# Kernel tuning notes

Measured on AMD Instinct MI355X. Metric: run time of the kernel, lower is better.

## Reference

```python
import jax, jax.numpy as jnp
import numpy as np

B, S, H = 1, 2048, 2048
NH = 16
HS = H // NH  # 128
NEG = -65504.0  # fp16 min used as additive mask value


def setup_inputs() -> dict:
    key = jax.random.key(0)
    k1, k2, k3, k4, k5 = jax.random.split(key, 5)
    hidden_states = jax.random.normal(k1, (B, S, H), dtype=jnp.float32)
    # causal left-to-right mask: 1 where attention allowed
    ltor_mask = jnp.tril(jnp.ones((S, S), dtype=jnp.float32))[None, None, :, :]
    W_qkv = jax.random.normal(k2, (H, 3 * H), dtype=jnp.float32) * (1.0 / np.sqrt(H))
    b_qkv = jax.random.normal(k3, (3 * H,), dtype=jnp.float32) * 0.01
    W_dense = jax.random.normal(k4, (H, H), dtype=jnp.float32) * (1.0 / np.sqrt(H))
    b_dense = jax.random.normal(k5, (H,), dtype=jnp.float32) * 0.01
    return {"hidden_states": hidden_states, "ltor_mask": ltor_mask,
            "W_qkv": W_qkv, "b_qkv": b_qkv, "W_dense": W_dense, "b_dense": b_dense}


def reference(hidden_states, ltor_mask, W_qkv, b_qkv, W_dense, b_dense):
    b, s, h = hidden_states.shape
    # fused QKV projection, then split along last dim (matches split_tensor_along_last_dim)
    qkv = hidden_states @ W_qkv + b_qkv  # [b, s, 3h]
    q, k, v = jnp.split(qkv, 3, axis=-1)
    q = q.reshape(b, s, NH, HS)
    k = k.reshape(b, s, NH, HS)
    v = v.reshape(b, s, NH, HS)
    scale = 1.0 / np.sqrt(HS)  # softmax_scale=None -> 1/sqrt(headdim)
    scores = jnp.einsum('bqhd,bkhd->bhqk', q, k) * scale
    scores = scores + NEG * (1.0 - ltor_mask)  # additive mask, [b,1,s,s] broadcast over heads
    probs = jax.nn.softmax(scores, axis=-1)
    ctx = jnp.einsum('bhqk,bkhd->bqhd', probs, v).reshape(b, s, h)
    out = ctx @ W_dense + b_dense  # output_dropout is identity in eval
    return out
```

## Files before the change

### kernel.cpp

```cpp
#include <hip/hip_runtime.h>
#include <math.h>

#define S_LEN 2048
#define HDIM  2048
#define NHEAD 16
#define HSZ   128
#define H3    6144

typedef __attribute__((ext_vector_type(8))) short bf16x8;
typedef __attribute__((ext_vector_type(4))) float f32x4;

__device__ inline ushort f2bf(float f) {
    union { float f; unsigned u; } c; c.f = f;
    unsigned u = c.u;
    return (ushort)((u + 0x7fffu + ((u >> 16) & 1u)) >> 16);
}
__device__ inline ushort f2bf_trunc(float f) {
    union { float f; unsigned u; } c; c.f = f;
    return (ushort)(c.u >> 16);
}

__global__ __launch_bounds__(256) void prep(
    const float* __restrict__ X,    ushort* __restrict__ Xb,
    const float* __restrict__ Wqkv, ushort* __restrict__ Wqt,
    const float* __restrict__ Wd,   ushort* __restrict__ Wdt)
{
    __shared__ ushort t[64][66];
    const int bid = blockIdx.x;
    const int tid = threadIdx.x;

    if (bid < 4096) {
        int i = bid * 1024 + tid * 4;
        float4 v = *(const float4*)(X + i);
        ushort4 o;
        o.x = f2bf(v.x); o.y = f2bf(v.y); o.z = f2bf(v.z); o.w = f2bf(v.w);
        *(ushort4*)(Xb + i) = o;
        return;
    }

    const float* W; ushort* Wt; int K, N, n0, k0;
    if (bid < 7168) {
        const int b = bid - 4096;
        W = Wqkv; Wt = Wqt; K = HDIM; N = H3;
        n0 = (b % 96) * 64; k0 = (b / 96) * 64;
    } else {
        const int b = bid - 7168;
        W = Wd; Wt = Wdt; K = HDIM; N = HDIM;
        n0 = (b % 32) * 64; k0 = (b / 32) * 64;
    }
    const int tx = tid & 15;
    const int ty = tid >> 4;
    #pragma unroll
    for (int p = 0; p < 4; p++) {
        const int k = p * 16 + ty;
        float4 v = *(const float4*)(&W[(size_t)(k0 + k) * N + n0 + tx * 4]);
        t[k][tx * 4 + 0] = f2bf(v.x);
        t[k][tx * 4 + 1] = f2bf(v.y);
        t[k][tx * 4 + 2] = f2bf(v.z);
        t[k][tx * 4 + 3] = f2bf(v.w);
    }
    __syncthreads();
    #pragma unroll
    for (int p = 0; p < 4; p++) {
        const int n = p * 16 + ty;
        ushort4 o;
        o.x = t[tx * 4 + 0][n];
        o.y = t[tx * 4 + 1][n];
        o.z = t[tx * 4 + 2][n];
        o.w = t[tx * 4 + 3][n];
        *(ushort4*)(&Wt[(size_t)(n0 + n) * K + k0 + tx * 4]) = o;
    }
}

__global__ __launch_bounds__(256) void transpose_v(const ushort* __restrict__ qkvb,
                                                   ushort* __restrict__ Vtb) {
    __shared__ ushort t[64][66];
    const int s0 = blockIdx.x * 64;
    const int d0 = blockIdx.y * 64;
    const int tx = threadIdx.x & 15;
    const int ty = threadIdx.x >> 4;
    #pragma unroll
    for (int p = 0; p < 4; p++) {
        const int s = p * 16 + ty;
        ushort4 v = *(const ushort4*)(&qkvb[(size_t)(s0 + s) * H3 + 2 * HDIM + d0 + tx * 4]);
        *(ushort4*)(&t[s][tx * 4]) = v;
    }
    __syncthreads();
    #pragma unroll
    for (int p = 0; p < 4; p++) {
        const int d = p * 16 + ty;
        ushort4 o;
        o.x = t[tx * 4 + 0][d];
        o.y = t[tx * 4 + 1][d];
        o.z = t[tx * 4 + 2][d];
        o.w = t[tx * 4 + 3][d];
        *(ushort4*)(&Vtb[(size_t)(d0 + d) * S_LEN + s0 + tx * 4]) = o;
    }
}

__global__ __launch_bounds__(256, 2) void gemm_qkv_v4(
    const ushort* __restrict__ A, const ushort* __restrict__ Bt,
    const float* __restrict__ bias, ushort* __restrict__ Cb,
    int M, int N, int K)
{
    __shared__ __align__(16) ushort lds[2][128 * 64 + 192 * 64];

    const int tid  = threadIdx.x;
    const int m0   = blockIdx.y * 128;
    const int n0   = blockIdx.x * 192;
    const int w    = tid >> 6;
    const int wm   = w >> 1;
    const int wn   = w & 1;
    const int lane = tid & 63;
    const int quad = lane >> 4;
    const int l16  = lane & 15;

    const int rdsw = l16 & 7;

    f32x4 acc[4][6] = {};

    const int T = K / 64;

    auto stage = [&](int kt) {
        const int b  = kt & 1;
        const int k0 = kt * 64;
        #pragma unroll
        for (int r = 0; r < 4; r++) {
            const int c   = r * 256 + tid;
            const int row = c >> 3;
            const int csw = ((c & 7) ^ (row & 7)) * 8;
            const ushort* ga = A + (size_t)(m0 + row) * K + k0 + csw;
            __builtin_amdgcn_global_load_lds(
                (const __attribute__((address_space(1))) void*)ga,
                (__attribute__((address_space(3))) void*)(&lds[b][0] + c * 8), 16, 0, 0);
        }
        #pragma unroll
        for (int r = 0; r < 6; r++) {
            const int c   = r * 256 + tid;
            const int row = c >> 3;
            const int csw = ((c & 7) ^ (row & 7)) * 8;
            const ushort* gb = Bt + (size_t)(n0 + row) * K + k0 + csw;
            __builtin_amdgcn_global_load_lds(
                (const __attribute__((address_space(1))) void*)gb,
                (__attribute__((address_space(3))) void*)(&lds[b][8192] + c * 8), 16, 0, 0);
        }
    };

    stage(0);

    for (int u = 0; u < T; u++) {
        const int b = u & 1;
        if (u + 1 < T) {
            stage(u + 1);
            asm volatile("s_waitcnt vmcnt(10)" ::: "memory");
        } else {
            asm volatile("s_waitcnt vmcnt(0)" ::: "memory");
        }
        asm volatile("s_barrier" ::: "memory");

        const ushort* bA = &lds[b][0];
        const ushort* bB = &lds[b][8192];

        bf16x8 af[4][2], bq[6][2];
        #pragma unroll
        for (int i = 0; i < 4; i++)
            #pragma unroll
            for (int kc = 0; kc < 2; kc++)
                af[i][kc] = *(const bf16x8*)(bA + (wm * 64 + i * 16 + l16) * 64
                                               + ((((kc << 2) | quad) ^ rdsw) * 8));
        #pragma unroll
        for (int j = 0; j < 6; j++)
            #pragma unroll
            for (int kc = 0; kc < 2; kc++)
                bq[j][kc] = *(const bf16x8*)(bB + (wn * 96 + j * 16 + l16) * 64
                                               + ((((kc << 2) | quad) ^ rdsw) * 8));

        __builtin_amdgcn_s_setprio(1);
        #pragma unroll
        for (int i = 0; i < 4; i++)
            #pragma unroll
            for (int j = 0; j < 6; j++)
                #pragma unroll
                for (int kc = 0; kc < 2; kc++)
                    acc[i][j] = __builtin_amdgcn_mfma_f32_16x16x32_bf16(
                        af[i][kc], bq[j][kc], acc[i][j], 0, 0, 0);
        __builtin_amdgcn_s_setprio(0);

        asm volatile("s_waitcnt lgkmcnt(0)" ::: "memory");
        asm volatile("s_barrier" ::: "memory");
    }

    #pragma unroll
    for (int i = 0; i < 4; i++) {
        #pragma unroll
        for (int r = 0; r < 4; r++) {
            const int m = m0 + wm * 64 + i * 16 + quad * 4 + r;
            #pragma unroll
            for (int j = 0; j < 6; j++) {
                const int n = n0 + wn * 96 + j * 16 + l16;
                float v  = acc[i][j][r] + bias[n];
                float vp = __shfl_xor(v, 1, 64);
                unsigned both = (unsigned)f2bf(v) | ((unsigned)f2bf(vp) << 16);
                if ((l16 & 1) == 0)
                    *(unsigned*)(Cb + (size_t)m * N + n) = both;
            }
        }
    }
}

__global__ __launch_bounds__(256) void gemm_dense(
    const ushort* __restrict__ A, const ushort* __restrict__ Bt,
    const float* __restrict__ bias, float* __restrict__ C)
{
    __shared__ ushort sA[2 * 64 * 32];
    __shared__ ushort sB[2 * 128 * 32];

    const int tid  = threadIdx.x;
    const int m0   = blockIdx.y * 64;
    const int n0   = blockIdx.x * 128;
    const int w    = tid >> 6;
    const int lane = tid & 63;
    const int quad = lane >> 4;
    const int l16  = lane & 15;
    const int wr   = (w >> 1) * 32;
    const int wc   = (w & 1) * 64;

    f32x4 acc[2][4] = {};

    for (int k0 = 0; k0 < HDIM; k0 += 64) {
        #pragma unroll
        for (int iss = 0; iss < 2; iss++) {
            const int li  = iss * 256 + tid;
            const int c   = li >> 8;
            const int row = (li >> 2) & 63;
            const int kc  = (li & 3) * 8;
            const ushort* ga = A + (size_t)(m0 + row) * HDIM + k0 + c * 32 + kc;
            __builtin_amdgcn_global_load_lds(
                (const __attribute__((address_space(1))) void*)ga,
                (__attribute__((address_space(3))) void*)(sA + li * 8), 16, 0, 0);
        }
        #pragma unroll
        for (int iss = 0; iss < 4; iss++) {
            const int li  = iss * 256 + tid;
            const int c   = li >> 9;
            const int row = (li >> 2) & 127;
            const int kc  = (li & 3) * 8;
            const ushort* gb = Bt + (size_t)(n0 + row) * HDIM + k0 + c * 32 + kc;
            __builtin_amdgcn_global_load_lds(
                (const __attribute__((address_space(1))) void*)gb,
                (__attribute__((address_space(3))) void*)(sB + li * 8), 16, 0, 0);
        }
        __syncthreads();

        #pragma unroll
        for (int c = 0; c < 2; c++) {
            bf16x8 af[2], bq[4];
            #pragma unroll
            for (int i = 0; i < 2; i++)
                af[i] = *(const bf16x8*)(sA + c * 2048 + (wr + i * 16 + l16) * 32 + quad * 8);
            #pragma unroll
            for (int j = 0; j < 4; j++)
                bq[j] = *(const bf16x8*)(sB + c * 4096 + (wc + j * 16 + l16) * 32 + quad * 8);

            #pragma unroll
            for (int i = 0; i < 2; i++)
                #pragma unroll
                for (int j = 0; j < 4; j++)
                    acc[i][j] = __builtin_amdgcn_mfma_f32_16x16x32_bf16(
                        af[i], bq[j], acc[i][j], 0, 0, 0);
        }
        __syncthreads();
    }

    #pragma unroll
    for (int i = 0; i < 2; i++)
        #pragma unroll
        for (int r = 0; r < 4; r++) {
            const int m = m0 + wr + i * 16 + quad * 4 + r;
            #pragma unroll
            for (int j = 0; j < 4; j++) {
                const int n = n0 + wc + j * 16 + l16;
                C[(size_t)m * HDIM + n] = acc[i][j][r] + bias[n];
            }
        }
}

__global__ __launch_bounds__(256) void attn_split(
    const ushort* __restrict__ qkvb, const ushort* __restrict__ Vtb,
    float* __restrict__ po, float* __restrict__ ctxf)
{
    __shared__ __align__(16) ushort sK [2][64 * 128];
    __shared__ __align__(16) ushort sVt[2][128 * 64];
    __shared__ __align__(16) ushort Ps [4 * 1024];

    const int tid = threadIdx.x;
    const int bid = blockIdx.x;
    const int qt  = 31 - (bid >> 5);
    const int rem = bid & 31;
    const int h   = rem >> 1;
    const int sh  = rem & 1;
    const int nt  = qt + 1;
    const int h0  = (nt + 1) >> 1;
    const int ks  = sh ? h0 : 0;
    const int ke  = sh ? nt : h0;

    const int q0   = qt * 64;
    const int w    = tid >> 6;
    const int lane = tid & 63;
    const int quad = lane >> 4;
    const int l16  = lane & 15;
    const int qr0  = q0 + w * 16;

    const float scale = 0.08838834764831845f;

    bf16x8 qf[4];
    #pragma unroll
    for (int c = 0; c < 4; c++)
        qf[c] = *(const bf16x8*)(qkvb + (size_t)(qr0 + l16) * H3 + h * HSZ + c * 32 + quad * 8);

    f32x4 o[8] = {};
    float lsum[4] = {0.f, 0.f, 0.f, 0.f};

    const int skey = tid >> 2;
    const int sq8  = tid & 3;

    auto stage = [&](int kt, int b) {
        const int k0 = kt * 64;
        #pragma unroll
        for (int iss = 0; iss < 4; iss++) {
            const int li = iss * 256 + tid;
            const ushort* g = qkvb + (size_t)(k0 + skey) * H3 + HDIM + h * HSZ + iss * 32 + sq8 * 8;
            __builtin_amdgcn_global_load_lds(
                (const __attribute__((address_space(1))) void*)g,
                (__attribute__((address_space(3))) void*)(&sK[b][0] + li * 8), 16, 0, 0);
        }
        #pragma unroll
        for (int iss = 0; iss < 4; iss++) {
            const int li = iss * 256 + tid;
            const int c  = li >> 9;
            const int d  = (li >> 2) & 127;
            const ushort* g = Vtb + (size_t)(h * HSZ + d) * S_LEN + k0 + c * 32 + (li & 3) * 8;
            __builtin_amdgcn_global_load_lds(
                (const __attribute__((address_space(1))) void*)g,
                (__attribute__((address_space(3))) void*)(&sVt[b][0] + li * 8), 16, 0, 0);
        }
    };

    if (ks < ke) stage(ks, 0);
    const int wofs = w * 1024;

    for (int kt = ks; kt < ke; kt++) {
        const int b  = (kt - ks) & 1;
        const int k0 = kt * 64;

        if (kt + 1 < ke) {
            stage(kt + 1, b ^ 1);
            asm volatile("s_waitcnt vmcnt(8)" ::: "memory");
        } else {
            asm volatile("s_waitcnt vmcnt(0)" ::: "memory");
        }
        asm volatile("s_barrier" ::: "memory");

        const ushort* bK = &sK[b][0];
        const ushort* bV = &sVt[b][0];

        f32x4 sacc[4] = {};
        #pragma unroll
        for (int jt = 0; jt < 4; jt++)
            #pragma unroll
            for (int c = 0; c < 4; c++) {
                bf16x8 kf = *(const bf16x8*)(bK + c * 2048 + (jt * 16 + l16) * 32 + quad * 8);
                sacc[jt] = __builtin_amdgcn_mfma_f32_16x16x32_bf16(qf[c], kf, sacc[jt], 0, 0, 0);
            }

        float p[4][4];
        if (kt == qt) {
            #pragma unroll
            for (int jt = 0; jt < 4; jt++) {
                const int key = k0 + jt * 16 + l16;
                #pragma unroll
                for (int r = 0; r < 4; r++) {
                    float e = __expf(sacc[jt][r] * scale);
                    if (key > qr0 + quad * 4 + r) e = 0.f;
                    p[jt][r] = e;
                    lsum[r] += e;
                }
            }
        } else {
            #pragma unroll
            for (int jt = 0; jt < 4; jt++)
                #pragma unroll
                for (int r = 0; r < 4; r++) {
                    float e = __expf(sacc[jt][r] * scale);
                    p[jt][r] = e;
                    lsum[r] += e;
                }
        }

        #pragma unroll
        for (int jt = 0; jt < 4; jt++) {
            const int cpan = jt >> 1;
            const int lch  = (jt & 1) * 2 + (l16 >> 3);
            const int phys = lch ^ quad;
            #pragma unroll
            for (int r = 0; r < 4; r++) {
                const int row = quad * 4 + r;
                Ps[wofs + cpan * 512 + row * 32 + phys * 8 + (l16 & 7)] = f2bf_trunc(p[jt][r]);
            }
        }

        #pragma unroll
        for (int c = 0; c < 2; c++) {
            const int pph = quad ^ (l16 >> 2);
            bf16x8 pf = *(const bf16x8*)(Ps + wofs + c * 512 + l16 * 32 + pph * 8);
            #pragma unroll
            for (int ht = 0; ht < 8; ht++) {
                bf16x8 vf = *(const bf16x8*)(bV + c * 4096 + (ht * 16 + l16) * 32 + quad * 8);
                o[ht] = __builtin_amdgcn_mfma_f32_16x16x32_bf16(pf, vf, o[ht], 0, 0, 0);
            }
        }

        asm volatile("s_waitcnt lgkmcnt(0)" ::: "memory");
        asm volatile("s_barrier" ::: "memory");
    }

    float* poS = po + (size_t)sh * S_LEN * HDIM;

    #pragma unroll
    for (int r = 0; r < 4; r++) {
        float ls = lsum[r];
        #pragma unroll
        for (int off = 1; off < 16; off <<= 1)
            ls += __shfl_xor(ls, off, 64);
        const int row = qr0 + quad * 4 + r;
        if (l16 == 0)
            ctxf[(size_t)row * 1024 + sh * 16 + h] = ls;
    }
    #pragma unroll
    for (int ht = 0; ht < 8; ht++) {
        #pragma unroll
        for (int r = 0; r < 4; r++) {
            const int row = qr0 + quad * 4 + r;
            float v  = o[ht][r];
            float vp = __shfl_xor(v, 1, 64);
            if ((l16 & 1) == 0) {
                float2 t; t.x = v; t.y = vp;
                *(float2*)(poS + (size_t)row * HDIM + h * HSZ + ht * 16 + l16) = t;
            }
        }
    }
}

__global__ __launch_bounds__(256) void attn_combine(
    const float* __restrict__ po, const float* __restrict__ ctxf,
    ushort* __restrict__ ctxb)
{
    __shared__ float linv[16];
    const int row = blockIdx.x;
    const int tid = threadIdx.x;

    if (tid < 16) {
        float l0 = ctxf[(size_t)row * 1024 + tid];
        float l1 = ctxf[(size_t)row * 1024 + 16 + tid];
        linv[tid] = 1.0f / (l0 + l1);
    }
    __syncthreads();

    const float* r0 = po + (size_t)row * HDIM;
    const float* r1 = po + (size_t)S_LEN * HDIM + (size_t)row * HDIM;
    const int c0 = tid * 8;
    const float s = linv[c0 >> 7];

    float4 a0 = *(const float4*)(r0 + c0);
    float4 b0 = *(const float4*)(r1 + c0);
    float4 a1 = *(const float4*)(r0 + c0 + 4);
    float4 b1 = *(const float4*)(r1 + c0 + 4);

    ushort4 u0, u1;
    u0.x = f2bf((a0.x + b0.x) * s); u0.y = f2bf((a0.y + b0.y) * s);
    u0.z = f2bf((a0.z + b0.z) * s); u0.w = f2bf((a0.w + b0.w) * s);
    u1.x = f2bf((a1.x + b1.x) * s); u1.y = f2bf((a1.y + b1.y) * s);
    u1.z = f2bf((a1.z + b1.z) * s); u1.w = f2bf((a1.w + b1.w) * s);

    *(ushort4*)(ctxb + (size_t)row * HDIM + c0)     = u0;
    *(ushort4*)(ctxb + (size_t)row * HDIM + c0 + 4) = u1;
}

extern "C" void kernel_launch(void* const* d_in, const int* in_sizes, int n_in,
                              void* d_out, int out_size, void* d_ws, size_t ws_size,
                              hipStream_t stream) {
    const float* X    = (const float*)d_in[0];
    const float* Wqkv = (const float*)d_in[2];
    const float* bqkv = (const float*)d_in[3];
    const float* Wd   = (const float*)d_in[4];
    const float* bd   = (const float*)d_in[5];
    float* out = (float*)d_out;

    ushort* Xb   = (ushort*)d_ws;
    ushort* Wqt  = Xb   + (size_t)S_LEN * HDIM;
    ushort* Wdt  = Wqt  + (size_t)H3 * HDIM;
    ushort* ctxb = Wdt  + (size_t)HDIM * HDIM;
    ushort* qkvb = ctxb + (size_t)S_LEN * HDIM;
    ushort* Vtb  = qkvb + (size_t)S_LEN * H3;

    float* po   = (float*)d_ws;
    float* ctxf = (float*)ctxb;

    dim3 blk(256);

    prep<<<dim3(8192), blk, 0, stream>>>(X, Xb, Wqkv, Wqt, Wd, Wdt);

    gemm_qkv_v4<<<dim3(H3 / 192, S_LEN / 128), blk, 0, stream>>>(
        Xb, Wqt, bqkv, qkvb, S_LEN, H3, HDIM);

    transpose_v<<<dim3(S_LEN / 64, HDIM / 64), blk, 0, stream>>>(qkvb, Vtb);

    attn_split<<<dim3(1024), blk, 0, stream>>>(qkvb, Vtb, po, ctxf);

    attn_combine<<<dim3(S_LEN), blk, 0, stream>>>(po, ctxf, ctxb);

    gemm_dense<<<dim3(HDIM / 128, S_LEN / 64), blk, 0, stream>>>(
        ctxb, Wdt, bd, out);
}
```

Measured before the change: 268.1 us.

## Retile QKV GEMM to 128x128x32 and pipeline dense GEMM with swizzled double-buffered LDS

The QKV projection GEMM moves from 128x192 tiles with K-step 64 to 128x128 tiles with K-step 32, using less LDS and a higher occupancy hint so more blocks (384 instead of 256) spread across CUs. The output dense GEMM is rewritten in the same style as the QKV kernel: double-buffered LDS with XOR swizzle, prefetch of the next K tile before compute, and a partial vmcnt wait in place of full __syncthreads around each load. The aim is better CU fill and less LDS bank conflict and load stall. The cost is lower per-block data reuse and twice as many barrier iterations in the QKV GEMM.

After: 272.7 us. About the same (+1.7%).

```diff
diff --git a/kernel.cpp b/kernel.cpp
--- a/kernel.cpp
+++ b/kernel.cpp
@@ -98,16 +98,16 @@
     }
 }
 
-__global__ __launch_bounds__(256, 2) void gemm_qkv_v4(
+__global__ __launch_bounds__(256, 3) void gemm_qkv_v5(
     const ushort* __restrict__ A, const ushort* __restrict__ Bt,
     const float* __restrict__ bias, ushort* __restrict__ Cb,
     int M, int N, int K)
 {
-    __shared__ __align__(16) ushort lds[2][128 * 64 + 192 * 64];
+    __shared__ __align__(16) ushort lds[2][128 * 32 + 128 * 32];
 
     const int tid  = threadIdx.x;
     const int m0   = blockIdx.y * 128;
-    const int n0   = blockIdx.x * 192;
+    const int n0   = blockIdx.x * 128;
     const int w    = tid >> 6;
     const int wm   = w >> 1;
     const int wn   = w & 1;
@@ -115,34 +115,137 @@
     const int quad = lane >> 4;
     const int l16  = lane & 15;
 
+    const int rdsw = l16 & 3;
+
+    f32x4 acc[4][4] = {};
+
+    const int T = K / 32;
+
+    auto stage = [&](int kt) {
+        const int b  = kt & 1;
+        const int k0 = kt * 32;
+        #pragma unroll
+        for (int r = 0; r < 2; r++) {
+            const int c   = r * 256 + tid;
+            const int row = c >> 2;
+            const int csw = ((c & 3) ^ (row & 3)) * 8;
+            const ushort* ga = A + (size_t)(m0 + row) * K + k0 + csw;
+            __builtin_amdgcn_global_load_lds(
+                (const __attribute__((address_space(1))) void*)ga,
+                (__attribute__((address_space(3))) void*)(&lds[b][0] + c * 8), 16, 0, 0);
+        }
+        #pragma unroll
+        for (int r = 0; r < 2; r++) {
+            const int c   = r * 256 + tid;
+            const int row = c >> 2;
+            const int csw = ((c & 3) ^ (row & 3)) * 8;
+            const ushort* gb = Bt + (size_t)(n0 + row) * K + k0 + csw;
+            __builtin_amdgcn_global_load_lds(
+                (const __attribute__((address_space(1))) void*)gb,
+                (__attribute__((address_space(3))) void*)(&lds[b][4096] + c * 8), 16, 0, 0);
+        }
+    };
+
+    stage(0);
+
+    for (int u = 0; u < T; u++) {
+        const int b = u & 1;
+        if (u + 1 < T) {
+            stage(u + 1);
+            asm volatile("s_waitcnt vmcnt(4)" ::: "memory");
+        } else {
+            asm volatile("s_waitcnt vmcnt(0)" ::: "memory");
+        }
+        asm volatile("s_barrier" ::: "memory");
+
+        const ushort* bA = &lds[b][0];
+        const ushort* bB = &lds[b][4096];
+
+        bf16x8 af[4], bq[4];
+        #pragma unroll
+        for (int i = 0; i < 4; i++)
+            af[i] = *(const bf16x8*)(bA + (wm * 64 + i * 16 + l16) * 32
+                                       + ((quad ^ rdsw) * 8));
+        #pragma unroll
+        for (int j = 0; j < 4; j++)
+            bq[j] = *(const bf16x8*)(bB + (wn * 64 + j * 16 + l16) * 32
+                                       + ((quad ^ rdsw) * 8));
+
+        __builtin_amdgcn_s_setprio(1);
+        #pragma unroll
+        for (int i = 0; i < 4; i++)
+            #pragma unroll
+            for (int j = 0; j < 4; j++)
+                acc[i][j] = __builtin_amdgcn_mfma_f32_16x16x32_bf16(
+                    af[i], bq[j], acc[i][j], 0, 0, 0);
+        __builtin_amdgcn_s_setprio(0);
+
+        asm volatile("s_waitcnt lgkmcnt(0)" ::: "memory");
+        asm volatile("s_barrier" ::: "memory");
+    }
+
+    #pragma unroll
+    for (int i = 0; i < 4; i++) {
+        #pragma unroll
+        for (int r = 0; r < 4; r++) {
+            const int m = m0 + wm * 64 + i * 16 + quad * 4 + r;
+            #pragma unroll
+            for (int j = 0; j < 4; j++) {
+                const int n = n0 + wn * 64 + j * 16 + l16;
+                float v  = acc[i][j][r] + bias[n];
+                float vp = __shfl_xor(v, 1, 64);
+                unsigned both = (unsigned)f2bf(v) | ((unsigned)f2bf(vp) << 16);
+                if ((l16 & 1) == 0)
+                    *(unsigned*)(Cb + (size_t)m * N + n) = both;
+            }
+        }
+    }
+}
+
+__global__ __launch_bounds__(256, 2) void gemm_dense_v2(
+    const ushort* __restrict__ A, const ushort* __restrict__ Bt,
+    const float* __restrict__ bias, float* __restrict__ C)
+{
+    __shared__ __align__(16) ushort lds[2][64 * 64 + 128 * 64];
+
+    const int tid  = threadIdx.x;
+    const int m0   = blockIdx.y * 64;
+    const int n0   = blockIdx.x * 128;
+    const int w    = tid >> 6;
+    const int wm   = w >> 1;
+    const int wn   = w & 1;
+    const int lane = tid & 63;
+    const int quad = lane >> 4;
+    const int l16  = lane & 15;
+
     const int rdsw = l16 & 7;
 
-    f32x4 acc[4][6] = {};
-
-    const int T = K / 64;
+    f32x4 acc[2][4] = {};
+
+    const int T = HDIM / 64;
 
     auto stage = [&](int kt) {
         const int b  = kt & 1;
         const int k0 = kt * 64;
+        #pragma unroll
+        for (int r = 0; r < 2; r++) {
+            const int c   = r * 256 + tid;
+            const int row = c >> 3;
+            const int csw = ((c & 7) ^ (row & 7)) * 8;
+            const ushort* ga = A + (size_t)(m0 + row) * HDIM + k0 + csw;
+            __builtin_amdgcn_global_load_lds(
+                (const __attribute__((address_space(1))) void*)ga,
+                (__attribute__((address_space(3))) void*)(&lds[b][0] + c * 8), 16, 0, 0);
+        }
         #pragma unroll
         for (int r = 0; r < 4; r++) {
             const int c   = r * 256 + tid;
             const int row = c >> 3;
             const int csw = ((c & 7) ^ (row & 7)) * 8;
-            const ushort* ga = A + (size_t)(m0 + row) * K + k0 + csw;
-            __builtin_amdgcn_global_load_lds(
-                (const __attribute__((address_space(1))) void*)ga,
-                (__attribute__((address_space(3))) void*)(&lds[b][0] + c * 8), 16, 0, 0);
-        }
-        #pragma unroll
-        for (int r = 0; r < 6; r++) {
-            const int c   = r * 256 + tid;
-            const int row = c >> 3;
-            const int csw = ((c & 7) ^ (row & 7)) * 8;
-            const ushort* gb = Bt + (size_t)(n0 + row) * K + k0 + csw;
+            const ushort* gb = Bt + (size_t)(n0 + row) * HDIM + k0 + csw;
             __builtin_amdgcn_global_load_lds(
                 (const __attribute__((address_space(1))) void*)gb,
-                (__attribute__((address_space(3))) void*)(&lds[b][8192] + c * 8), 16, 0, 0);
+                (__attribute__((address_space(3))) void*)(&lds[b][4096] + c * 8), 16, 0, 0);
         }
     };
 
@@ -152,34 +255,34 @@
         const int b = u & 1;
         if (u + 1 < T) {
             stage(u + 1);
-            asm volatile("s_waitcnt vmcnt(10)" ::: "memory");
+            asm volatile("s_waitcnt vmcnt(6)" ::: "memory");
         } else {
             asm volatile("s_waitcnt vmcnt(0)" ::: "memory");
         }
         asm volatile("s_barrier" ::: "memory");
 
         const ushort* bA = &lds[b][0];
-        const ushort* bB = &lds[b][8192];
-
-        bf16x8 af[4][2], bq[6][2];
-        #pragma unroll
-        for (int i = 0; i < 4; i++)
+        const ushort* bB = &lds[b][4096];
+
+        bf16x8 af[2][2], bq[4][2];
+        #pragma unroll
+        for (int i = 0; i < 2; i++)
             #pragma unroll
             for (int kc = 0; kc < 2; kc++)
-                af[i][kc] = *(const bf16x8*)(bA + (wm * 64 + i * 16 + l16) * 64
+                af[i][kc] = *(const bf16x8*)(bA + (wm * 32 + i * 16 + l16) * 64
                                                + ((((kc << 2) | quad) ^ rdsw) * 8));
         #pragma unroll
-        for (int j = 0; j < 6; j++)
+        for (int j = 0; j < 4; j++)
             #pragma unroll
             for (int kc = 0; kc < 2; kc++)
-                bq[j][kc] = *(const bf16x8*)(bB + (wn * 96 + j * 16 + l16) * 64
+                bq[j][kc] = *(const bf16x8*)(bB + (wn * 64 + j * 16 + l16) * 64
                                                + ((((kc << 2) | quad) ^ rdsw) * 8));
 
         __builtin_amdgcn_s_setprio(1);
         #pragma unroll
-        for (int i = 0; i < 4; i++)
-            #pragma unroll
-            for (int j = 0; j < 6; j++)
+        for (int i = 0; i < 2; i++)
+            #pragma unroll
+            for (int j = 0; j < 4; j++)
                 #pragma unroll
                 for (int kc = 0; kc < 2; kc++)
                     acc[i][j] = __builtin_amdgcn_mfma_f32_16x16x32_bf16(
@@ -191,95 +294,13 @@
     }
 
     #pragma unroll
-    for (int i = 0; i < 4; i++) {
+    for (int i = 0; i < 2; i++)
         #pragma unroll
         for (int r = 0; r < 4; r++) {
-            const int m = m0 + wm * 64 + i * 16 + quad * 4 + r;
-            #pragma unroll
-            for (int j = 0; j < 6; j++) {
-                const int n = n0 + wn * 96 + j * 16 + l16;
-                float v  = acc[i][j][r] + bias[n];
-                float vp = __shfl_xor(v, 1, 64);
-                unsigned both = (unsigned)f2bf(v) | ((unsigned)f2bf(vp) << 16);
-                if ((l16 & 1) == 0)
-                    *(unsigned*)(Cb + (size_t)m * N + n) = both;
-            }
-        }
-    }
-}
-
-__global__ __launch_bounds__(256) void gemm_dense(
-    const ushort* __restrict__ A, const ushort* __restrict__ Bt,
-    const float* __restrict__ bias, float* __restrict__ C)
-{
-    __shared__ ushort sA[2 * 64 * 32];
-    __shared__ ushort sB[2 * 128 * 32];
-
-    const int tid  = threadIdx.x;
-    const int m0   = blockIdx.y * 64;
-    const int n0   = blockIdx.x * 128;
-    const int w    = tid >> 6;
-    const int lane = tid & 63;
-    const int quad = lane >> 4;
-    const int l16  = lane & 15;
-    const int wr   = (w >> 1) * 32;
-    const int wc   = (w & 1) * 64;
-
-    f32x4 acc[2][4] = {};
-
-    for (int k0 = 0; k0 < HDIM; k0 += 64) {
-        #pragma unroll
-        for (int iss = 0; iss < 2; iss++) {
-            const int li  = iss * 256 + tid;
-            const int c   = li >> 8;
-            const int row = (li >> 2) & 63;
-            const int kc  = (li & 3) * 8;
-            const ushort* ga = A + (size_t)(m0 + row) * HDIM + k0 + c * 32 + kc;
-            __builtin_amdgcn_global_load_lds(
-                (const __attribute__((address_space(1))) void*)ga,
-                (__attribute__((address_space(3))) void*)(sA + li * 8), 16, 0, 0);
-        }
-        #pragma unroll
-        for (int iss = 0; iss < 4; iss++) {
-            const int li  = iss * 256 + tid;
-            const int c   = li >> 9;
-            const int row = (li >> 2) & 127;
-            const int kc  = (li & 3) * 8;
-            const ushort* gb = Bt + (size_t)(n0 + row) * HDIM + k0 + c * 32 + kc;
-            __builtin_amdgcn_global_load_lds(
-                (const __attribute__((address_space(1))) void*)gb,
-                (__attribute__((address_space(3))) void*)(sB + li * 8), 16, 0, 0);
-        }
-        __syncthreads();
-
-        #pragma unroll
-        for (int c = 0; c < 2; c++) {
-            bf16x8 af[2], bq[4];
-            #pragma unroll
-            for (int i = 0; i < 2; i++)
-                af[i] = *(const bf16x8*)(sA + c * 2048 + (wr + i * 16 + l16) * 32 + quad * 8);
-            #pragma unroll
-            for (int j = 0; j < 4; j++)
-                bq[j] = *(const bf16x8*)(sB + c * 4096 + (wc + j * 16 + l16) * 32 + quad * 8);
-
-            #pragma unroll
-            for (int i = 0; i < 2; i++)
-                #pragma unroll
-                for (int j = 0; j < 4; j++)
-                    acc[i][j] = __builtin_amdgcn_mfma_f32_16x16x32_bf16(
-                        af[i], bq[j], acc[i][j], 0, 0, 0);
-        }
-        __syncthreads();
-    }
-
-    #pragma unroll
-    for (int i = 0; i < 2; i++)
-        #pragma unroll
-        for (int r = 0; r < 4; r++) {
-            const int m = m0 + wr + i * 16 + quad * 4 + r;
+            const int m = m0 + wm * 32 + i * 16 + quad * 4 + r;
             #pragma unroll
             for (int j = 0; j < 4; j++) {
-                const int n = n0 + wc + j * 16 + l16;
+                const int n = n0 + wn * 64 + j * 16 + l16;
                 C[(size_t)m * HDIM + n] = acc[i][j][r] + bias[n];
             }
         }
@@ -510,7 +531,7 @@
 
     prep<<<dim3(8192), blk, 0, stream>>>(X, Xb, Wqkv, Wqt, Wd, Wdt);
 
-    gemm_qkv_v4<<<dim3(H3 / 192, S_LEN / 128), blk, 0, stream>>>(
+    gemm_qkv_v5<<<dim3(H3 / 128, S_LEN / 128), blk, 0, stream>>>(
         Xb, Wqt, bqkv, qkvb, S_LEN, H3, HDIM);
 
     transpose_v<<<dim3(S_LEN / 64, HDIM / 64), blk, 0, stream>>>(qkvb, Vtb);
@@ -519,6 +540,6 @@
 
     attn_combine<<<dim3(S_LEN), blk, 0, stream>>>(po, ctxf, ctxb);
 
-    gemm_dense<<<dim3(HDIM / 128, S_LEN / 64), blk, 0, stream>>>(
+    gemm_dense_v2<<<dim3(HDIM / 128, S_LEN / 64), blk, 0, stream>>>(
         ctxb, Wdt, bd, out);
 }
```
